# Kernel optimization log

Measured on AMD Instinct MI355X. Metric: run time of the kernel, lower is better.

Reference implementation:

```python
import jax, jax.numpy as jnp
import numpy as np


def _vieta_pell_basis(x, degree):
    # Iterative recurrence: V0 = 2, V1 = x, Vn = x*V_{n-1} + V_{n-2}
    basis = [2.0 * jnp.ones_like(x), x]
    for _ in range(2, degree + 1):
        basis.append(x * basis[-1] + basis[-2])
    return jnp.stack(basis[: degree + 1], axis=-1)  # [b, i, d+1]


def setup_inputs() -> dict:
    key = jax.random.key(0)
    k1, k2 = jax.random.split(key)
    batch, input_dim, output_dim, degree = 4096, 1024, 1024, 8
    x = jax.random.normal(k1, (batch, input_dim), dtype=jnp.float32)
    std = 1.0 / (input_dim * (degree + 1))
    vp_coeffs = jax.random.normal(k2, (input_dim, output_dim, degree + 1), dtype=jnp.float32) * std
    return {"x": x, "vp_coeffs": vp_coeffs}


def reference(x, vp_coeffs):
    degree = vp_coeffs.shape[-1] - 1
    xt = jnp.tanh(x)  # [b, i]
    vp_basis = _vieta_pell_basis(xt, degree)  # [b, i, d+1]
    y = jnp.einsum("bid,iod->bo", vp_basis, vp_coeffs)
    return y
```

## Files before the change

kernel.cpp:

```cpp
#include <hip/hip_runtime.h>
#include <hip/hip_bf16.h>

typedef unsigned short u16;
typedef unsigned int   u32;
typedef unsigned long long u64;

#define BATCH 4096
#define IDIM  1024
#define ODIM  1024
#define NDEG  9
#define KTOT  (IDIM * NDEG)

#define BM 128
#define BN 128
#define BKK 64

typedef __attribute__((ext_vector_type(8))) short short8_t;
typedef __attribute__((ext_vector_type(4))) float f32x4;

__device__ __forceinline__ u16 f2bf(float f) {
    union { float f; u32 u; } v; v.f = f;
    u32 r = v.u + 0x7FFFu + ((v.u >> 16) & 1u);
    return (u16)(r >> 16);
}
__device__ __forceinline__ u32 pack2bf(float lo, float hi) {
    return (u32)f2bf(lo) | ((u32)f2bf(hi) << 16);
}

__device__ __forceinline__ void gl_lds16(const u16* g, u16* l) {
    __builtin_amdgcn_global_load_lds(
        (const __attribute__((address_space(1))) void*)g,
        (__attribute__((address_space(3))) void*)l,
        16, 0, 0);
}

#define PB_TI 128
#define PB_TO 8
#define PB_J  (PB_TO * NDEG)
#define PB_LS 132

#define NB_B   1024
#define NB_A   8192

__global__ void prep_kernel(const float* __restrict__ x,
                            const float* __restrict__ c,
                            u16* __restrict__ A, u16* __restrict__ Bt) {
    __shared__ u16 lds[PB_J * PB_LS];
    const int bb  = blockIdx.x;
    const int tid = threadIdx.x;

    if (bb < NB_B) {
        const int i0 = (bb & 7) * PB_TI;
        const int o0 = (bb >> 3) * PB_TO;
        const float* src = c + (size_t)i0 * (ODIM * NDEG) + (size_t)o0 * NDEG;
#pragma unroll
        for (int t = 0; t < 36; ++t) {
            int f  = t * 256 + tid;
            int ii = f / PB_J;
            int j  = f - ii * PB_J;
            float v = src[(size_t)ii * (ODIM * NDEG) + j];
            lds[j * PB_LS + ii] = f2bf(v);
        }
        __syncthreads();
#pragma unroll
        for (int t = 0; t < 9; ++t) {
            int g   = t * 256 + tid;
            int j   = g >> 5;
            int ii4 = (g & 31) << 2;
            int o   = j / NDEG;
            int d   = j - o * NDEG;
            u64 v = *(const u64*)(lds + j * PB_LS + ii4);
            *(u64*)(Bt + (size_t)(o0 + o) * KTOT + d * 1024 + i0 + ii4) = v;
        }
    } else {
        int t  = (bb - NB_B) * 256 + tid;
        int b  = t >> 9;
        int i2 = (t & 511) << 1;
        float2 xv = ((const float2*)x)[t];
        float t0 = tanhf(xv.x), t1 = tanhf(xv.y);
        u32* dst = (u32*)(A + (size_t)b * KTOT + i2);
        float a0 = 2.0f, a1 = 2.0f;
        float b0 = t0,  b1 = t1;
        dst[0]   = pack2bf(2.0f, 2.0f);
        dst[512] = pack2bf(t0, t1);
#pragma unroll
        for (int d = 2; d < NDEG; ++d) {
            float n0 = t0 * b0 + a0;
            float n1 = t1 * b1 + a1;
            dst[(size_t)d * 512] = pack2bf(n0, n1);
            a0 = b0; b0 = n0; a1 = b1; b1 = n1;
        }
    }
}

__global__ __launch_bounds__(256, 2)
void gemm_kernel(const u16* __restrict__ A, const u16* __restrict__ B,
                 float* __restrict__ P) {
    __shared__ __align__(16) u16 ldsA[BM * BKK];
    __shared__ __align__(16) u16 ldsB[BN * BKK];

    const int tid  = threadIdx.x;
    const int lane = tid & 63;
    const int wave = tid >> 6;
    const int quad = lane >> 4;
    const int l15  = lane & 15;
    const int wm   = wave & 1;
    const int wn   = wave >> 1;

    const int bid = blockIdx.x;
    const int xcd = bid & 7;
    const int loc = bid >> 3;
    const int z   = xcd >> 2;
    const int bm  = ((xcd & 3) << 3) | (loc >> 3);
    const int bn  = loc & 7;
    const int kStart = z * (KTOT / 2);
    float* C = P + (size_t)z * BATCH * ODIM;

    const u16* ga[4]; const u16* gb[4];
    u16* la[4]; u16* lb[4];
#pragma unroll
    for (int t = 0; t < 4; ++t) {
        int s  = t * 256 + tid;
        int r  = s >> 3;
        int sc = (s & 7) ^ (r & 7);
        ga[t] = A + (size_t)(bm * BM + r) * KTOT + kStart + sc * 8;
        gb[t] = B + (size_t)(bn * BN + r) * KTOT + kStart + sc * 8;
        la[t] = ldsA + s * 8;
        lb[t] = ldsB + s * 8;
    }

    f32x4 acc[4][4];
#pragma unroll
    for (int mt = 0; mt < 4; ++mt)
#pragma unroll
        for (int nt = 0; nt < 4; ++nt)
            acc[mt][nt] = (f32x4){0.f, 0.f, 0.f, 0.f};

    const int nIter = (KTOT / 2) / BKK;
    for (int it = 0; it < nIter; ++it) {
#pragma unroll
        for (int t = 0; t < 4; ++t) gl_lds16(ga[t], la[t]);
#pragma unroll
        for (int t = 0; t < 4; ++t) gl_lds16(gb[t], lb[t]);
        __syncthreads();

#pragma unroll
        for (int kk = 0; kk < 2; ++kk) {
            short8_t af[4], bfg[4];
#pragma unroll
            for (int mt = 0; mt < 4; ++mt) {
                int row = wm * 64 + mt * 16 + l15;
                int pc  = (kk * 4 + quad) ^ (row & 7);
                af[mt] = *(const short8_t*)(ldsA + (row * 8 + pc) * 8);
            }
#pragma unroll
            for (int nt = 0; nt < 4; ++nt) {
                int row = wn * 64 + nt * 16 + l15;
                int pc  = (kk * 4 + quad) ^ (row & 7);
                bfg[nt] = *(const short8_t*)(ldsB + (row * 8 + pc) * 8);
            }
#pragma unroll
            for (int mt = 0; mt < 4; ++mt)
#pragma unroll
                for (int nt = 0; nt < 4; ++nt)
                    acc[mt][nt] = __builtin_amdgcn_mfma_f32_16x16x32_bf16(
                        af[mt], bfg[nt], acc[mt][nt], 0, 0, 0);
        }
        __syncthreads();

#pragma unroll
        for (int t = 0; t < 4; ++t) { ga[t] += BKK; gb[t] += BKK; }
    }

#pragma unroll
    for (int mt = 0; mt < 4; ++mt) {
#pragma unroll
        for (int nt = 0; nt < 4; ++nt) {
            int row0 = bm * BM + wm * 64 + mt * 16 + quad * 4;
            int col  = bn * BN + wn * 64 + nt * 16 + l15;
#pragma unroll
            for (int r = 0; r < 4; ++r)
                C[(size_t)(row0 + r) * ODIM + col] = acc[mt][nt][r];
        }
    }
}

__global__ void reduce_kernel(const float* __restrict__ P, float* __restrict__ out) {
    int t = blockIdx.x * 256 + threadIdx.x;
    f32x4 a = ((const f32x4*)P)[t];
    f32x4 b = ((const f32x4*)(P + (size_t)BATCH * ODIM))[t];
    ((f32x4*)out)[t] = a + b;
}

extern "C" void kernel_launch(void* const* d_in, const int* in_sizes, int n_in,
                              void* d_out, int out_size, void* d_ws, size_t ws_size,
                              hipStream_t stream) {
    const float* x      = (const float*)d_in[0];
    const float* coeffs = (const float*)d_in[1];
    float* out = (float*)d_out;

    u16* A  = (u16*)d_ws;
    u16* Bt = A + (size_t)BATCH * KTOT;
    float* P = (float*)(Bt + (size_t)ODIM * KTOT);

    prep_kernel<<<NB_B + NB_A, 256, 0, stream>>>(x, coeffs, A, Bt);
    gemm_kernel<<<512, 256, 0, stream>>>(A, Bt, P);
    reduce_kernel<<<BATCH * ODIM / 1024, 256, 0, stream>>>(P, out);
}
```

Before: 187.3 us.

## Use single-wave 64x64 GEMM blocks with double-buffered async LDS loads

Replaces the 4-wave 128x128 GEMM block with a single 64-lane wave that computes a 64x64 tile. The wave double-buffers its LDS tiles and prefetches the next K-slice while computing the current one, using vmcnt waits instead of __syncthreads. The intent is to remove block-level barriers and to overlap global-to-LDS traffic with MFMA work. In exchange there is no operand reuse across waves, so each block loads twice the A/B bytes per FLOP, and correctness depends on the hand-coded waitcnt values.

```diff
diff --git a/kernel.cpp b/kernel.cpp
--- a/kernel.cpp
+++ b/kernel.cpp
@@ -10,13 +10,13 @@
 #define ODIM  1024
 #define NDEG  9
 #define KTOT  (IDIM * NDEG)
-
-#define BM 128
-#define BN 128
-#define BKK 64
+#define KHALF (KTOT / 2)
 
 typedef __attribute__((ext_vector_type(8))) short short8_t;
 typedef __attribute__((ext_vector_type(4))) float f32x4;
+
+#define WAIT_VM16 0x4F70
+#define WAIT_VM0  0x0F70
 
 __device__ __forceinline__ u16 f2bf(float f) {
     union { float f; u32 u; } v; v.f = f;
@@ -93,40 +93,32 @@
     }
 }
 
-__global__ __launch_bounds__(256, 2)
+__global__ __launch_bounds__(64, 2)
 void gemm_kernel(const u16* __restrict__ A, const u16* __restrict__ B,
                  float* __restrict__ P) {
-    __shared__ __align__(16) u16 ldsA[BM * BKK];
-    __shared__ __align__(16) u16 ldsB[BN * BKK];
-
-    const int tid  = threadIdx.x;
-    const int lane = tid & 63;
-    const int wave = tid >> 6;
+    __shared__ __align__(16) u16 lds[2][2][4096];
+
+    const int lane = threadIdx.x;
     const int quad = lane >> 4;
     const int l15  = lane & 15;
-    const int wm   = wave & 1;
-    const int wn   = wave >> 1;
 
     const int bid = blockIdx.x;
     const int xcd = bid & 7;
     const int loc = bid >> 3;
-    const int z   = xcd >> 2;
-    const int bm  = ((xcd & 3) << 3) | (loc >> 3);
-    const int bn  = loc & 7;
-    const int kStart = z * (KTOT / 2);
-    float* C = P + (size_t)z * BATCH * ODIM;
-
-    const u16* ga[4]; const u16* gb[4];
-    u16* la[4]; u16* lb[4];
-#pragma unroll
-    for (int t = 0; t < 4; ++t) {
-        int s  = t * 256 + tid;
+    const int z   = loc >> 7;
+    const int lv  = loc & 127;
+    const int bm  = ((xcd & 3) << 4) | (lv & 15);
+    const int bn  = ((xcd >> 2) << 3) | (lv >> 4);
+    const int kStart = z * KHALF;
+
+    const u16* ga[8]; const u16* gb[8];
+#pragma unroll
+    for (int i = 0; i < 8; ++i) {
+        int s  = i * 64 + lane;
         int r  = s >> 3;
         int sc = (s & 7) ^ (r & 7);
-        ga[t] = A + (size_t)(bm * BM + r) * KTOT + kStart + sc * 8;
-        gb[t] = B + (size_t)(bn * BN + r) * KTOT + kStart + sc * 8;
-        la[t] = ldsA + s * 8;
-        lb[t] = ldsB + s * 8;
+        ga[i] = A + (size_t)(bm * 64 + r) * KTOT + kStart + sc * 8;
+        gb[i] = B + (size_t)(bn * 64 + r) * KTOT + kStart + sc * 8;
     }
 
     f32x4 acc[4][4];
@@ -136,28 +128,43 @@
         for (int nt = 0; nt < 4; ++nt)
             acc[mt][nt] = (f32x4){0.f, 0.f, 0.f, 0.f};
 
-    const int nIter = (KTOT / 2) / BKK;
+#pragma unroll
+    for (int i = 0; i < 8; ++i) gl_lds16(ga[i], &lds[0][0][i * 512 + lane * 8]);
+#pragma unroll
+    for (int i = 0; i < 8; ++i) gl_lds16(gb[i], &lds[0][1][i * 512 + lane * 8]);
+
+    const int nIter = KHALF / 64;
     for (int it = 0; it < nIter; ++it) {
-#pragma unroll
-        for (int t = 0; t < 4; ++t) gl_lds16(ga[t], la[t]);
-#pragma unroll
-        for (int t = 0; t < 4; ++t) gl_lds16(gb[t], lb[t]);
-        __syncthreads();
+        const int cur = it & 1;
+        if (it + 1 < nIter) {
+            const int off = (it + 1) * 64;
+            const int nxt = cur ^ 1;
+#pragma unroll
+            for (int i = 0; i < 8; ++i)
+                gl_lds16(ga[i] + off, &lds[nxt][0][i * 512 + lane * 8]);
+#pragma unroll
+            for (int i = 0; i < 8; ++i)
+                gl_lds16(gb[i] + off, &lds[nxt][1][i * 512 + lane * 8]);
+            __builtin_amdgcn_s_waitcnt(WAIT_VM16);
+        } else {
+            __builtin_amdgcn_s_waitcnt(WAIT_VM0);
+        }
+        __builtin_amdgcn_sched_barrier(0);
 
 #pragma unroll
         for (int kk = 0; kk < 2; ++kk) {
             short8_t af[4], bfg[4];
 #pragma unroll
             for (int mt = 0; mt < 4; ++mt) {
-                int row = wm * 64 + mt * 16 + l15;
+                int row = mt * 16 + l15;
                 int pc  = (kk * 4 + quad) ^ (row & 7);
-                af[mt] = *(const short8_t*)(ldsA + (row * 8 + pc) * 8);
+                af[mt] = *(const short8_t*)(&lds[cur][0][(row * 8 + pc) * 8]);
             }
 #pragma unroll
             for (int nt = 0; nt < 4; ++nt) {
-                int row = wn * 64 + nt * 16 + l15;
+                int row = nt * 16 + l15;
                 int pc  = (kk * 4 + quad) ^ (row & 7);
-                bfg[nt] = *(const short8_t*)(ldsB + (row * 8 + pc) * 8);
+                bfg[nt] = *(const short8_t*)(&lds[cur][1][(row * 8 + pc) * 8]);
             }
 #pragma unroll
             for (int mt = 0; mt < 4; ++mt)
@@ -166,18 +173,15 @@
                     acc[mt][nt] = __builtin_amdgcn_mfma_f32_16x16x32_bf16(
                         af[mt], bfg[nt], acc[mt][nt], 0, 0, 0);
         }
-        __syncthreads();
-
-#pragma unroll
-        for (int t = 0; t < 4; ++t) { ga[t] += BKK; gb[t] += BKK; }
-    }
-
+    }
+
+    float* C = P + (size_t)z * BATCH * ODIM;
 #pragma unroll
     for (int mt = 0; mt < 4; ++mt) {
 #pragma unroll
         for (int nt = 0; nt < 4; ++nt) {
-            int row0 = bm * BM + wm * 64 + mt * 16 + quad * 4;
-            int col  = bn * BN + wn * 64 + nt * 16 + l15;
+            int row0 = bm * 64 + mt * 16 + quad * 4;
+            int col  = bn * 64 + nt * 16 + l15;
 #pragma unroll
             for (int r = 0; r < 4; ++r)
                 C[(size_t)(row0 + r) * ODIM + col] = acc[mt][nt][r];
@@ -204,6 +208,6 @@
     float* P = (float*)(Bt + (size_t)ODIM * KTOT);
 
     prep_kernel<<<NB_B + NB_A, 256, 0, stream>>>(x, coeffs, A, Bt);
-    gemm_kernel<<<512, 256, 0, stream>>>(A, Bt, P);
+    gemm_kernel<<<2048, 64, 0, stream>>>(A, Bt, P);
     reduce_kernel<<<BATCH * ODIM / 1024, 256, 0, stream>>>(P, out);
 }
```

After: 217.7 us. 1.16x slower.

## Generate Vieta-Pell basis on the fly inside GEMM instead of materializing A

Applied to the files above, without the earlier changes.

Removes the bf16 basis matrix A (4096x9216) from the prep kernel and instead computes tanh and the Vieta-Pell recurrence inside the GEMM, writing the bf16 basis tile directly into LDS. Each split-K half handles a degree range per 64-column input window, recomputing tanh per block. This eliminates a large global write and read of A, but adds redundant tanh and recurrence work across the N-dimension blocks and serializes A-tile generation with the MFMA loop.

```diff
diff --git a/kernel.cpp b/kernel.cpp
--- a/kernel.cpp
+++ b/kernel.cpp
@@ -11,12 +11,9 @@
 #define NDEG  9
 #define KTOT  (IDIM * NDEG)
 
-#define BM 128
-#define BN 128
-#define BKK 64
-
 typedef __attribute__((ext_vector_type(8))) short short8_t;
 typedef __attribute__((ext_vector_type(4))) float f32x4;
+typedef __attribute__((ext_vector_type(4))) u32   u32x4;
 
 __device__ __forceinline__ u16 f2bf(float f) {
     union { float f; u32 u; } v; v.f = f;
@@ -39,65 +36,39 @@
 #define PB_J  (PB_TO * NDEG)
 #define PB_LS 132
 
-#define NB_B   1024
-#define NB_A   8192
-
-__global__ void prep_kernel(const float* __restrict__ x,
-                            const float* __restrict__ c,
-                            u16* __restrict__ A, u16* __restrict__ Bt) {
+__global__ void prep_kernel(const float* __restrict__ c, u16* __restrict__ Bt) {
     __shared__ u16 lds[PB_J * PB_LS];
     const int bb  = blockIdx.x;
     const int tid = threadIdx.x;
-
-    if (bb < NB_B) {
-        const int i0 = (bb & 7) * PB_TI;
-        const int o0 = (bb >> 3) * PB_TO;
-        const float* src = c + (size_t)i0 * (ODIM * NDEG) + (size_t)o0 * NDEG;
-#pragma unroll
-        for (int t = 0; t < 36; ++t) {
-            int f  = t * 256 + tid;
-            int ii = f / PB_J;
-            int j  = f - ii * PB_J;
-            float v = src[(size_t)ii * (ODIM * NDEG) + j];
-            lds[j * PB_LS + ii] = f2bf(v);
-        }
-        __syncthreads();
-#pragma unroll
-        for (int t = 0; t < 9; ++t) {
-            int g   = t * 256 + tid;
-            int j   = g >> 5;
-            int ii4 = (g & 31) << 2;
-            int o   = j / NDEG;
-            int d   = j - o * NDEG;
-            u64 v = *(const u64*)(lds + j * PB_LS + ii4);
-            *(u64*)(Bt + (size_t)(o0 + o) * KTOT + d * 1024 + i0 + ii4) = v;
-        }
-    } else {
-        int t  = (bb - NB_B) * 256 + tid;
-        int b  = t >> 9;
-        int i2 = (t & 511) << 1;
-        float2 xv = ((const float2*)x)[t];
-        float t0 = tanhf(xv.x), t1 = tanhf(xv.y);
-        u32* dst = (u32*)(A + (size_t)b * KTOT + i2);
-        float a0 = 2.0f, a1 = 2.0f;
-        float b0 = t0,  b1 = t1;
-        dst[0]   = pack2bf(2.0f, 2.0f);
-        dst[512] = pack2bf(t0, t1);
-#pragma unroll
-        for (int d = 2; d < NDEG; ++d) {
-            float n0 = t0 * b0 + a0;
-            float n1 = t1 * b1 + a1;
-            dst[(size_t)d * 512] = pack2bf(n0, n1);
-            a0 = b0; b0 = n0; a1 = b1; b1 = n1;
-        }
+    const int i0 = (bb & 7) * PB_TI;
+    const int o0 = (bb >> 3) * PB_TO;
+    const float* src = c + (size_t)i0 * (ODIM * NDEG) + (size_t)o0 * NDEG;
+#pragma unroll
+    for (int t = 0; t < 36; ++t) {
+        int f  = t * 256 + tid;
+        int ii = f / PB_J;
+        int j  = f - ii * PB_J;
+        float v = src[(size_t)ii * (ODIM * NDEG) + j];
+        lds[j * PB_LS + ii] = f2bf(v);
+    }
+    __syncthreads();
+#pragma unroll
+    for (int t = 0; t < 9; ++t) {
+        int g   = t * 256 + tid;
+        int j   = g >> 5;
+        int ii4 = (g & 31) << 2;
+        int o   = j / NDEG;
+        int d   = j - o * NDEG;
+        u64 v = *(const u64*)(lds + j * PB_LS + ii4);
+        *(u64*)(Bt + (size_t)(o0 + o) * KTOT + d * 1024 + i0 + ii4) = v;
     }
 }
 
 __global__ __launch_bounds__(256, 2)
-void gemm_kernel(const u16* __restrict__ A, const u16* __restrict__ B,
+void gemm_kernel(const float* __restrict__ X, const u16* __restrict__ B,
                  float* __restrict__ P) {
-    __shared__ __align__(16) u16 ldsA[BM * BKK];
-    __shared__ __align__(16) u16 ldsB[BN * BKK];
+    __shared__ __align__(16) u16 ldsA[128 * 64];
+    __shared__ __align__(16) u16 ldsB[128 * 64];
 
     const int tid  = threadIdx.x;
     const int lane = tid & 63;
@@ -113,21 +84,20 @@
     const int z   = xcd >> 2;
     const int bm  = ((xcd & 3) << 3) | (loc >> 3);
     const int bn  = loc & 7;
-    const int kStart = z * (KTOT / 2);
-    float* C = P + (size_t)z * BATCH * ODIM;
-
-    const u16* ga[4]; const u16* gb[4];
-    u16* la[4]; u16* lb[4];
+
+    const u16* gb[4]; u16* lb[4];
 #pragma unroll
     for (int t = 0; t < 4; ++t) {
         int s  = t * 256 + tid;
         int r  = s >> 3;
         int sc = (s & 7) ^ (r & 7);
-        ga[t] = A + (size_t)(bm * BM + r) * KTOT + kStart + sc * 8;
-        gb[t] = B + (size_t)(bn * BN + r) * KTOT + kStart + sc * 8;
-        la[t] = ldsA + s * 8;
+        gb[t] = B + (size_t)(bn * 128 + r) * KTOT + sc * 8;
         lb[t] = ldsB + s * 8;
     }
+
+    const int pr = tid >> 1;
+    const int ph = tid & 1;
+    const float* xrow = X + (size_t)(bm * 128 + pr) * IDIM + ph * 32;
 
     f32x4 acc[4][4];
 #pragma unroll
@@ -136,48 +106,108 @@
         for (int nt = 0; nt < 4; ++nt)
             acc[mt][nt] = (f32x4){0.f, 0.f, 0.f, 0.f};
 
-    const int nIter = (KTOT / 2) / BKK;
-    for (int it = 0; it < nIter; ++it) {
-#pragma unroll
-        for (int t = 0; t < 4; ++t) gl_lds16(ga[t], la[t]);
-#pragma unroll
-        for (int t = 0; t < 4; ++t) gl_lds16(gb[t], lb[t]);
-        __syncthreads();
-
-#pragma unroll
-        for (int kk = 0; kk < 2; ++kk) {
-            short8_t af[4], bfg[4];
-#pragma unroll
-            for (int mt = 0; mt < 4; ++mt) {
-                int row = wm * 64 + mt * 16 + l15;
-                int pc  = (kk * 4 + quad) ^ (row & 7);
-                af[mt] = *(const short8_t*)(ldsA + (row * 8 + pc) * 8);
+    for (int iw = 0; iw < 16; ++iw) {
+        float tv[32];
+        const f32x4* xp = (const f32x4*)(xrow + iw * 64);
+#pragma unroll
+        for (int q = 0; q < 8; ++q) {
+            f32x4 v = xp[q];
+            tv[q * 4 + 0] = tanhf(v[0]);
+            tv[q * 4 + 1] = tanhf(v[1]);
+            tv[q * 4 + 2] = tanhf(v[2]);
+            tv[q * 4 + 3] = tanhf(v[3]);
+        }
+
+        float Vp[32], Vc[32];
+        int dlo, dhi;
+        if (z == 0) {
+            dlo = 0; dhi = (iw < 8) ? 4 : 3;
+#pragma unroll
+            for (int e = 0; e < 32; ++e) { Vp[e] = 2.0f; Vc[e] = tv[e]; }
+        } else {
+            dlo = (iw < 8) ? 5 : 4; dhi = 8;
+#pragma unroll
+            for (int e = 0; e < 32; ++e) {
+                float V2 = tv[e] * tv[e] + 2.0f;
+                float V3 = tv[e] * V2 + tv[e];
+                if (iw >= 8) { Vp[e] = V2; Vc[e] = V3; }
+                else { Vp[e] = V3; Vc[e] = tv[e] * V3 + V2; }
             }
-#pragma unroll
-            for (int nt = 0; nt < 4; ++nt) {
-                int row = wn * 64 + nt * 16 + l15;
-                int pc  = (kk * 4 + quad) ^ (row & 7);
-                bfg[nt] = *(const short8_t*)(ldsB + (row * 8 + pc) * 8);
+        }
+
+        for (int d = dlo; d <= dhi; ++d) {
+            const int koff = d * 1024 + iw * 64;
+#pragma unroll
+            for (int t = 0; t < 4; ++t) gl_lds16(gb[t] + koff, lb[t]);
+
+            if (d == 0) {
+                u32x4 w = (u32x4){0x40004000u, 0x40004000u, 0x40004000u, 0x40004000u};
+#pragma unroll
+                for (int cc = 0; cc < 4; ++cc) {
+                    int pc = (ph * 4 + cc) ^ (pr & 7);
+                    *(u32x4*)(ldsA + (pr * 8 + pc) * 8) = w;
+                }
+            } else if (d == 1) {
+#pragma unroll
+                for (int cc = 0; cc < 4; ++cc) {
+                    int pc = (ph * 4 + cc) ^ (pr & 7);
+                    u32x4 w;
+#pragma unroll
+                    for (int j = 0; j < 4; ++j)
+                        w[j] = pack2bf(tv[cc * 8 + j * 2], tv[cc * 8 + j * 2 + 1]);
+                    *(u32x4*)(ldsA + (pr * 8 + pc) * 8) = w;
+                }
+            } else {
+#pragma unroll
+                for (int e = 0; e < 32; ++e) {
+                    float n = tv[e] * Vc[e] + Vp[e];
+                    Vp[e] = Vc[e]; Vc[e] = n;
+                }
+#pragma unroll
+                for (int cc = 0; cc < 4; ++cc) {
+                    int pc = (ph * 4 + cc) ^ (pr & 7);
+                    u32x4 w;
+#pragma unroll
+                    for (int j = 0; j < 4; ++j)
+                        w[j] = pack2bf(Vc[cc * 8 + j * 2], Vc[cc * 8 + j * 2 + 1]);
+                    *(u32x4*)(ldsA + (pr * 8 + pc) * 8) = w;
+                }
             }
-#pragma unroll
-            for (int mt = 0; mt < 4; ++mt)
-#pragma unroll
-                for (int nt = 0; nt < 4; ++nt)
-                    acc[mt][nt] = __builtin_amdgcn_mfma_f32_16x16x32_bf16(
-                        af[mt], bfg[nt], acc[mt][nt], 0, 0, 0);
-        }
-        __syncthreads();
-
-#pragma unroll
-        for (int t = 0; t < 4; ++t) { ga[t] += BKK; gb[t] += BKK; }
-    }
-
+            __syncthreads();
+
+#pragma unroll
+            for (int kk = 0; kk < 2; ++kk) {
+                short8_t af[4], bfg[4];
+#pragma unroll
+                for (int mt = 0; mt < 4; ++mt) {
+                    int row = wm * 64 + mt * 16 + l15;
+                    int pc  = (kk * 4 + quad) ^ (row & 7);
+                    af[mt] = *(const short8_t*)(ldsA + (row * 8 + pc) * 8);
+                }
+#pragma unroll
+                for (int nt = 0; nt < 4; ++nt) {
+                    int row = wn * 64 + nt * 16 + l15;
+                    int pc  = (kk * 4 + quad) ^ (row & 7);
+                    bfg[nt] = *(const short8_t*)(ldsB + (row * 8 + pc) * 8);
+                }
+#pragma unroll
+                for (int mt = 0; mt < 4; ++mt)
+#pragma unroll
+                    for (int nt = 0; nt < 4; ++nt)
+                        acc[mt][nt] = __builtin_amdgcn_mfma_f32_16x16x32_bf16(
+                            af[mt], bfg[nt], acc[mt][nt], 0, 0, 0);
+            }
+            __syncthreads();
+        }
+    }
+
+    float* C = P + (size_t)z * BATCH * ODIM;
 #pragma unroll
     for (int mt = 0; mt < 4; ++mt) {
 #pragma unroll
         for (int nt = 0; nt < 4; ++nt) {
-            int row0 = bm * BM + wm * 64 + mt * 16 + quad * 4;
-            int col  = bn * BN + wn * 64 + nt * 16 + l15;
+            int row0 = bm * 128 + wm * 64 + mt * 16 + quad * 4;
+            int col  = bn * 128 + wn * 64 + nt * 16 + l15;
 #pragma unroll
             for (int r = 0; r < 4; ++r)
                 C[(size_t)(row0 + r) * ODIM + col] = acc[mt][nt][r];
@@ -199,11 +229,10 @@
     const float* coeffs = (const float*)d_in[1];
     float* out = (float*)d_out;
 
-    u16* A  = (u16*)d_ws;
-    u16* Bt = A + (size_t)BATCH * KTOT;
+    u16* Bt = (u16*)d_ws;
     float* P = (float*)(Bt + (size_t)ODIM * KTOT);
 
-    prep_kernel<<<NB_B + NB_A, 256, 0, stream>>>(x, coeffs, A, Bt);
-    gemm_kernel<<<512, 256, 0, stream>>>(A, Bt, P);
+    prep_kernel<<<1024, 256, 0, stream>>>(coeffs, Bt);
+    gemm_kernel<<<512, 256, 0, stream>>>(x, Bt, P);
     reduce_kernel<<<BATCH * ODIM / 1024, 256, 0, stream>>>(P, out);
 }
```

Result: slower. 317.0 us (+69.2%).

## Fold constant degree-zero basis term into per-output bias, shrink GEMM K

Applied to the files above, without the earlier changes.

Because V0 is the constant 2, its contribution becomes 2 times the sum over inputs of the degree-0 coefficients, which is independent of the batch. The prep kernel computes these per-output sums with LDS atomics and writes partial sums per input tile, and the reduce kernel adds them to the result. Dropping the degree-0 slice shrinks the GEMM K dimension from 9216 to 8192, cutting GEMM work and the A/B workspace by about a ninth. In exchange it adds shared-memory atomics in prep and eight extra bias reads per output vector in reduce, and the bias is now summed in fp32 where the GEMM used bf16.

```diff
diff --git a/kernel.cpp b/kernel.cpp
--- a/kernel.cpp
+++ b/kernel.cpp
@@ -9,11 +9,8 @@
 #define IDIM  1024
 #define ODIM  1024
 #define NDEG  9
-#define KTOT  (IDIM * NDEG)
-
-#define BM 128
-#define BN 128
-#define BKK 64
+#define KA    8192
+#define KAH   (KA / 2)
 
 typedef __attribute__((ext_vector_type(8))) short short8_t;
 typedef __attribute__((ext_vector_type(4))) float f32x4;
@@ -44,8 +41,10 @@
 
 __global__ void prep_kernel(const float* __restrict__ x,
                             const float* __restrict__ c,
-                            u16* __restrict__ A, u16* __restrict__ Bt) {
+                            u16* __restrict__ A, u16* __restrict__ Bt,
+                            float* __restrict__ Pr) {
     __shared__ u16 lds[PB_J * PB_LS];
+    __shared__ float r1s[PB_TO];
     const int bb  = blockIdx.x;
     const int tid = threadIdx.x;
 
@@ -53,6 +52,8 @@
         const int i0 = (bb & 7) * PB_TI;
         const int o0 = (bb >> 3) * PB_TO;
         const float* src = c + (size_t)i0 * (ODIM * NDEG) + (size_t)o0 * NDEG;
+        if (tid < PB_TO) r1s[tid] = 0.0f;
+        __syncthreads();
 #pragma unroll
         for (int t = 0; t < 36; ++t) {
             int f  = t * 256 + tid;
@@ -60,6 +61,9 @@
             int j  = f - ii * PB_J;
             float v = src[(size_t)ii * (ODIM * NDEG) + j];
             lds[j * PB_LS + ii] = f2bf(v);
+            int o = j / NDEG;
+            int d = j - o * NDEG;
+            if (d == 0) atomicAdd(&r1s[o], v);
         }
         __syncthreads();
 #pragma unroll
@@ -69,25 +73,28 @@
             int ii4 = (g & 31) << 2;
             int o   = j / NDEG;
             int d   = j - o * NDEG;
-            u64 v = *(const u64*)(lds + j * PB_LS + ii4);
-            *(u64*)(Bt + (size_t)(o0 + o) * KTOT + d * 1024 + i0 + ii4) = v;
-        }
+            if (d != 0) {
+                u64 v = *(const u64*)(lds + j * PB_LS + ii4);
+                *(u64*)(Bt + (size_t)(o0 + o) * KA + (d - 1) * 1024 + i0 + ii4) = v;
+            }
+        }
+        if (tid < PB_TO)
+            Pr[(size_t)(bb & 7) * ODIM + o0 + tid] = r1s[tid];
     } else {
         int t  = (bb - NB_B) * 256 + tid;
         int b  = t >> 9;
         int i2 = (t & 511) << 1;
         float2 xv = ((const float2*)x)[t];
         float t0 = tanhf(xv.x), t1 = tanhf(xv.y);
-        u32* dst = (u32*)(A + (size_t)b * KTOT + i2);
+        u32* dst = (u32*)(A + (size_t)b * KA + i2);
         float a0 = 2.0f, a1 = 2.0f;
         float b0 = t0,  b1 = t1;
-        dst[0]   = pack2bf(2.0f, 2.0f);
-        dst[512] = pack2bf(t0, t1);
+        dst[0] = pack2bf(t0, t1);
 #pragma unroll
         for (int d = 2; d < NDEG; ++d) {
             float n0 = t0 * b0 + a0;
             float n1 = t1 * b1 + a1;
-            dst[(size_t)d * 512] = pack2bf(n0, n1);
+            dst[(size_t)(d - 1) * 512] = pack2bf(n0, n1);
             a0 = b0; b0 = n0; a1 = b1; b1 = n1;
         }
     }
@@ -96,8 +103,8 @@
 __global__ __launch_bounds__(256, 2)
 void gemm_kernel(const u16* __restrict__ A, const u16* __restrict__ B,
                  float* __restrict__ P) {
-    __shared__ __align__(16) u16 ldsA[BM * BKK];
-    __shared__ __align__(16) u16 ldsB[BN * BKK];
+    __shared__ __align__(16) u16 ldsA[128 * 64];
+    __shared__ __align__(16) u16 ldsB[128 * 64];
 
     const int tid  = threadIdx.x;
     const int lane = tid & 63;
@@ -113,8 +120,7 @@
     const int z   = xcd >> 2;
     const int bm  = ((xcd & 3) << 3) | (loc >> 3);
     const int bn  = loc & 7;
-    const int kStart = z * (KTOT / 2);
-    float* C = P + (size_t)z * BATCH * ODIM;
+    const int kStart = z * KAH;
 
     const u16* ga[4]; const u16* gb[4];
     u16* la[4]; u16* lb[4];
@@ -123,8 +129,8 @@
         int s  = t * 256 + tid;
         int r  = s >> 3;
         int sc = (s & 7) ^ (r & 7);
-        ga[t] = A + (size_t)(bm * BM + r) * KTOT + kStart + sc * 8;
-        gb[t] = B + (size_t)(bn * BN + r) * KTOT + kStart + sc * 8;
+        ga[t] = A + (size_t)(bm * 128 + r) * KA + kStart + sc * 8;
+        gb[t] = B + (size_t)(bn * 128 + r) * KA + kStart + sc * 8;
         la[t] = ldsA + s * 8;
         lb[t] = ldsB + s * 8;
     }
@@ -136,7 +142,7 @@
         for (int nt = 0; nt < 4; ++nt)
             acc[mt][nt] = (f32x4){0.f, 0.f, 0.f, 0.f};
 
-    const int nIter = (KTOT / 2) / BKK;
+    const int nIter = KAH / 64;
     for (int it = 0; it < nIter; ++it) {
 #pragma unroll
         for (int t = 0; t < 4; ++t) gl_lds16(ga[t], la[t]);
@@ -169,15 +175,16 @@
         __syncthreads();
 
 #pragma unroll
-        for (int t = 0; t < 4; ++t) { ga[t] += BKK; gb[t] += BKK; }
-    }
-
+        for (int t = 0; t < 4; ++t) { ga[t] += 64; gb[t] += 64; }
+    }
+
+    float* C = P + (size_t)z * BATCH * ODIM;
 #pragma unroll
     for (int mt = 0; mt < 4; ++mt) {
 #pragma unroll
         for (int nt = 0; nt < 4; ++nt) {
-            int row0 = bm * BM + wm * 64 + mt * 16 + quad * 4;
-            int col  = bn * BN + wn * 64 + nt * 16 + l15;
+            int row0 = bm * 128 + wm * 64 + mt * 16 + quad * 4;
+            int col  = bn * 128 + wn * 64 + nt * 16 + l15;
 #pragma unroll
             for (int r = 0; r < 4; ++r)
                 C[(size_t)(row0 + r) * ODIM + col] = acc[mt][nt][r];
@@ -185,11 +192,18 @@
     }
 }
 
-__global__ void reduce_kernel(const float* __restrict__ P, float* __restrict__ out) {
-    int t = blockIdx.x * 256 + threadIdx.x;
+__global__ void reduce_kernel(const float* __restrict__ P,
+                              const float* __restrict__ Pr,
+                              float* __restrict__ out) {
+    int t  = blockIdx.x * 256 + threadIdx.x;
+    int o4 = t & 255;
     f32x4 a = ((const f32x4*)P)[t];
-    f32x4 b = ((const f32x4*)(P + (size_t)BATCH * ODIM))[t];
-    ((f32x4*)out)[t] = a + b;
+    a += ((const f32x4*)(P + (size_t)BATCH * ODIM))[t];
+    f32x4 r = (f32x4){0.f, 0.f, 0.f, 0.f};
+#pragma unroll
+    for (int blk = 0; blk < 8; ++blk)
+        r += ((const f32x4*)Pr)[blk * 256 + o4];
+    ((f32x4*)out)[t] = a + r + r;
 }
 
 extern "C" void kernel_launch(void* const* d_in, const int* in_sizes, int n_in,
@@ -199,11 +213,12 @@
     const float* coeffs = (const float*)d_in[1];
     float* out = (float*)d_out;
 
-    u16* A  = (u16*)d_ws;
-    u16* Bt = A + (size_t)BATCH * KTOT;
-    float* P = (float*)(Bt + (size_t)ODIM * KTOT);
-
-    prep_kernel<<<NB_B + NB_A, 256, 0, stream>>>(x, coeffs, A, Bt);
+    u16*   A  = (u16*)d_ws;
+    u16*   Bt = A + (size_t)BATCH * KA;
+    float* Pr = (float*)(Bt + (size_t)ODIM * KA);
+    float* P  = Pr + 8 * ODIM;
+
+    prep_kernel<<<NB_B + NB_A, 256, 0, stream>>>(x, coeffs, A, Bt, Pr);
     gemm_kernel<<<512, 256, 0, stream>>>(A, Bt, P);
-    reduce_kernel<<<BATCH * ODIM / 1024, 256, 0, stream>>>(P, out);
-}
+    reduce_kernel<<<BATCH * ODIM / 1024, 256, 0, stream>>>(P, Pr, out);
+}
```

New measurement: 190.7 us. No clear change (+1.8%).
